# Kernel tuning notes

Hardware: AMD Instinct MI355X
Metric: run time of the kernel (lower is better)

## Reference

```python
import jax, jax.numpy as jnp
import numpy as np

B, S, D = 4, 2048, 768
H, E = 12, 64  # num_heads, head_size


def setup_inputs() -> dict:
    key = jax.random.key(0)
    ks = jax.random.split(key, 9)
    sd = 1.0 / np.sqrt(D)
    return {
        "x": jax.random.normal(ks[0], (B, S, D), dtype=jnp.float32),
        "Wq": jax.random.normal(ks[1], (H, D, E), dtype=jnp.float32) * sd,
        "bq": jax.random.normal(ks[2], (H, E), dtype=jnp.float32) * 0.02,
        "Wk": jax.random.normal(ks[3], (H, D, E), dtype=jnp.float32) * sd,
        "bk": jax.random.normal(ks[4], (H, E), dtype=jnp.float32) * 0.02,
        "Wv": jax.random.normal(ks[5], (H, D, E), dtype=jnp.float32) * sd,
        "bv": jax.random.normal(ks[6], (H, E), dtype=jnp.float32) * 0.02,
        "Wp": jax.random.normal(ks[7], (H * E, D), dtype=jnp.float32) * sd,
        "bp": jax.random.normal(ks[8], (D,), dtype=jnp.float32) * 0.02,
    }


def reference(x, Wq, bq, Wk, bk, Wv, bv, Wp, bp):
    # Batched multi-head QKV projections (replaces per-head Python loop)
    q = jnp.einsum("bsd,hde->bhse", x, Wq) + bq[None, :, None, :]
    k = jnp.einsum("bsd,hde->bhse", x, Wk) + bk[None, :, None, :]
    v = jnp.einsum("bsd,hde->bhse", x, Wv) + bv[None, :, None, :]
    scale = 1.0 / jnp.sqrt(jnp.asarray(E, dtype=x.dtype))
    # Full materialized attention matrix [B,H,S,S] as in the original module
    wei = jnp.einsum("bhqe,bhke->bhqk", q, k) * scale
    wei = jax.nn.softmax(wei, axis=-1)  # dropout=0 (eval) => identity
    out = jnp.einsum("bhqk,bhke->bhqe", wei, v)  # [B,H,S,E]
    # concat heads in head order then output projection
    out = out.transpose(0, 2, 1, 3).reshape(B, S, H * E)
    return out @ Wp + bp
```

## Files before the change

### kernel.cpp

```cpp
#include <hip/hip_runtime.h>
#include <cstddef>
#include <cstdint>

#define NB 4
#define NH 12
#define SQ 2048
#define DM 768
#define EH 64
#define MTOT (NB*SQ)
#define NQKV (NH*3*EH)

typedef __attribute__((ext_vector_type(8))) short short8;
typedef __attribute__((ext_vector_type(4))) float floatx4;

#define QSCALE 0.18033688011112042f

__device__ __forceinline__ unsigned short f2bf(float f) {
    unsigned int u = __float_as_uint(f);
    u += 0x7fffu + ((u >> 16) & 1u);
    return (unsigned short)(u >> 16);
}
__device__ __forceinline__ unsigned int pack_bf16_rhu(float lo, float hi) {
    unsigned int u0 = __float_as_uint(lo) + 0x8000u;
    unsigned int u1 = __float_as_uint(hi) + 0x8000u;
    return __builtin_amdgcn_perm(u1, u0, 0x07060302u);
}
__device__ __forceinline__ void gl_lds16(const void* g, void* l) {
    __builtin_amdgcn_global_load_lds(
        (const __attribute__((address_space(1))) unsigned int*)g,
        (__attribute__((address_space(3))) unsigned int*)l, 16, 0, 0);
}

#define CVT_A 1572864
#define CVT_B (CVT_A + 442368)
#define CVT_C (CVT_B + 147456)
#define CVT_D (CVT_C + 576)
__global__ __launch_bounds__(256) void convert_pack(
    const float* __restrict__ x,
    const float* __restrict__ Wq, const float* __restrict__ bq,
    const float* __restrict__ Wk, const float* __restrict__ bk,
    const float* __restrict__ Wv, const float* __restrict__ bv,
    const float* __restrict__ Wp,
    unsigned short* __restrict__ Xb, unsigned short* __restrict__ Wt,
    unsigned short* __restrict__ Wpt, float* __restrict__ bias_all)
{
    int t = blockIdx.x * 256 + threadIdx.x;
    if (t < CVT_A) {
        float4 v = ((const float4*)x)[t];
        ushort4 r; r.x = f2bf(v.x); r.y = f2bf(v.y); r.z = f2bf(v.z); r.w = f2bf(v.w);
        ((ushort4*)Xb)[t] = r;
    } else if (t < CVT_B) {
        int u = t - CVT_A;
        int n = u / 192, kc = (u % 192) * 4;
        int h = n / 192, rr = n % 192, wsel = rr >> 6, e = rr & 63;
        const float* W = (wsel == 0) ? Wq : ((wsel == 1) ? Wk : Wv);
        float sc = (wsel == 0) ? QSCALE : 1.0f;
        ushort4 r;
        r.x = f2bf(W[((size_t)h * DM + kc + 0) * EH + e] * sc);
        r.y = f2bf(W[((size_t)h * DM + kc + 1) * EH + e] * sc);
        r.z = f2bf(W[((size_t)h * DM + kc + 2) * EH + e] * sc);
        r.w = f2bf(W[((size_t)h * DM + kc + 3) * EH + e] * sc);
        ((ushort4*)Wt)[u] = r;
    } else if (t < CVT_C) {
        int u = t - CVT_B;
        int n = u / 192, kc = (u % 192) * 4;
        ushort4 r;
        r.x = f2bf(Wp[(size_t)(kc + 0) * DM + n]);
        r.y = f2bf(Wp[(size_t)(kc + 1) * DM + n]);
        r.z = f2bf(Wp[(size_t)(kc + 2) * DM + n]);
        r.w = f2bf(Wp[(size_t)(kc + 3) * DM + n]);
        ((ushort4*)Wpt)[u] = r;
    } else if (t < CVT_D) {
        int u = (t - CVT_C) * 4;
        #pragma unroll
        for (int j = 0; j < 4; j++) {
            int n = u + j;
            int h = n / 192, rr = n % 192, wsel = rr >> 6, e = rr & 63;
            const float* bs = (wsel == 0) ? bq : ((wsel == 1) ? bk : bv);
            bias_all[n] = bs[h * EH + e] * ((wsel == 0) ? QSCALE : 1.0f);
        }
    }
}

__global__ __launch_bounds__(256) void qkv_mfma(
    const unsigned short* __restrict__ Xb, const unsigned short* __restrict__ Wt,
    const float* __restrict__ bias_all,
    unsigned short* __restrict__ Qo, unsigned short* __restrict__ Kf,
    unsigned short* __restrict__ Vf)
{
    __shared__ unsigned short As[128 * 32];
    __shared__ unsigned short Bs[128 * 32];
    const int tid = threadIdx.x;
    const int w = tid >> 6, lane = tid & 63;
    const int l15 = lane & 15, quad = lane >> 4;
    const int wm = w & 1, wn = w >> 1;
    const int m0 = blockIdx.x * 128, n0 = blockIdx.y * 128;
    const int srow = w * 32 + (lane >> 2);
    const int pchunk = lane & 3;

    floatx4 acc[4][4];
    #pragma unroll
    for (int i = 0; i < 4; i++)
        #pragma unroll
        for (int j = 0; j < 4; j++) acc[i][j] = 0;

    for (int k0 = 0; k0 < DM; k0 += 32) {
        __syncthreads();
        #pragma unroll
        for (int c = 0; c < 2; c++) {
            int mr = srow + c * 16;
            int j = (pchunk - (mr >> 1)) & 3;
            gl_lds16(&Xb[(size_t)(m0 + mr) * DM + k0 + j * 8],
                     &As[w * 1024 + c * 512 + lane * 8]);
            gl_lds16(&Wt[(size_t)(n0 + mr) * DM + k0 + j * 8],
                     &Bs[w * 1024 + c * 512 + lane * 8]);
        }
        __syncthreads();
        short8 af[4], bf[4];
        #pragma unroll
        for (int mi = 0; mi < 4; mi++) {
            int row = wm * 64 + mi * 16 + l15;
            int pp = (quad + (row >> 1)) & 3;
            af[mi] = *(const short8*)&As[row * 32 + pp * 8];
        }
        #pragma unroll
        for (int ni = 0; ni < 4; ni++) {
            int row = wn * 64 + ni * 16 + l15;
            int pp = (quad + (row >> 1)) & 3;
            bf[ni] = *(const short8*)&Bs[row * 32 + pp * 8];
        }
        #pragma unroll
        for (int mi = 0; mi < 4; mi++)
            #pragma unroll
            for (int ni = 0; ni < 4; ni++)
                acc[mi][ni] = __builtin_amdgcn_mfma_f32_16x16x32_bf16(
                    af[mi], bf[ni], acc[mi][ni], 0, 0, 0);
    }

    const int bB = m0 >> 11;
    #pragma unroll
    for (int ni = 0; ni < 4; ni++) {
        int ntb = n0 + wn * 64 + ni * 16;
        int h = ntb / 192, rr = ntb % 192;
        int wsel = rr >> 6, e0 = rr & 63;
        float bv = bias_all[ntb + l15];
        size_t bhbase = ((size_t)bB * NH + h) * (SQ * EH);
        if (wsel == 0) {
            #pragma unroll
            for (int mi = 0; mi < 4; mi++) {
                int sb = (m0 & 2047) + wm * 64 + mi * 16 + quad * 4;
                #pragma unroll
                for (int r = 0; r < 4; r++)
                    Qo[bhbase + (size_t)(sb + r) * EH + e0 + l15] =
                        f2bf(acc[mi][ni][r] + bv);
            }
        } else if (wsel == 1) {
            int d = e0 + l15;
            int khalf = d >> 5, quad_d = (d >> 3) & 3, jj = d & 7;
            #pragma unroll
            for (int mi = 0; mi < 4; mi++) {
                int sb = (m0 & 2047) + wm * 64 + mi * 16 + quad * 4;
                int kbt = sb >> 6, nbk = (sb >> 4) & 3;
                size_t base = bhbase + (size_t)kbt * 4096 +
                    (size_t)(((nbk * 2 + khalf) * 64 + quad_d * 16 + (sb & 15))) * 8 + jj;
                #pragma unroll
                for (int r = 0; r < 4; r++)
                    Kf[base + r * 8] = f2bf(acc[mi][ni][r] + bv);
            }
        } else {
            int e = e0 + l15;
            int nbe = e >> 4;
            #pragma unroll
            for (int mi = 0; mi < 4; mi++) {
                int sb = (m0 & 2047) + wm * 64 + mi * 16 + quad * 4;
                int kbt = sb >> 6;
                int khk = (sb >> 5) & 1, qk = (sb >> 3) & 3, jb = sb & 7;
                size_t base = bhbase + (size_t)kbt * 4096 +
                    (size_t)(((nbe * 2 + khk) * 64 + qk * 16 + (e & 15))) * 8 + jb;
                ushort4 pk;
                pk.x = f2bf(acc[mi][ni][0] + bv);
                pk.y = f2bf(acc[mi][ni][1] + bv);
                pk.z = f2bf(acc[mi][ni][2] + bv);
                pk.w = f2bf(acc[mi][ni][3] + bv);
                *(ushort4*)&Vf[base] = pk;
            }
        }
    }
}

__global__ __launch_bounds__(256, 3) void attn_mfma(
    const unsigned short* __restrict__ Q, const unsigned short* __restrict__ Kf,
    const unsigned short* __restrict__ Vf, unsigned short* __restrict__ O)
{
    __shared__ unsigned short Ks[2][4096];
    __shared__ unsigned short Vs[2][4096];
    __shared__ unsigned short Pl[4][32 * 72];
    const int tid = threadIdx.x;
    const int w = tid >> 6, lane = tid & 63;
    const int l15 = lane & 15, quad = lane >> 4;
    const int bh = blockIdx.x;
    const int b = bh / NH, h = bh % NH;
    const int q0 = blockIdx.y * 128;
    unsigned short* Pw = &Pl[w][0];

    const unsigned short* Qb = Q + (size_t)bh * SQ * EH;
    const unsigned short* Kb = Kf + (size_t)bh * SQ * EH;
    const unsigned short* Vb = Vf + (size_t)bh * SQ * EH;

    short8 qf[2][2];
    #pragma unroll
    for (int qh = 0; qh < 2; qh++)
        #pragma unroll
        for (int kh = 0; kh < 2; kh++)
            qf[qh][kh] = *(const short8*)
                &Qb[(size_t)(q0 + w * 32 + qh * 16 + l15) * EH + kh * 32 + quad * 8];

    short8 ones;
    #pragma unroll
    for (int j = 0; j < 8; j++) ones[j] = (short)0x3F80;

    floatx4 o[2][4], l_acc[2];
    #pragma unroll
    for (int qh = 0; qh < 2; qh++) {
        l_acc[qh] = 0;
        #pragma unroll
        for (int nb = 0; nb < 4; nb++) o[qh][nb] = 0;
    }

    const int seg = w * 2;
    #pragma unroll
    for (int c = 0; c < 2; c++) {
        gl_lds16(&Kb[(seg + c) * 512 + lane * 8], &Ks[0][(seg + c) * 512 + lane * 8]);
        gl_lds16(&Vb[(seg + c) * 512 + lane * 8], &Vs[0][(seg + c) * 512 + lane * 8]);
    }

    #pragma unroll 2
    for (int kb = 0; kb < SQ / 64; kb++) {
        const int cur = kb & 1;
        __syncthreads();
        if (kb + 1 < SQ / 64) {
            const unsigned short* Kn = Kb + (size_t)(kb + 1) * 4096;
            const unsigned short* Vn = Vb + (size_t)(kb + 1) * 4096;
            #pragma unroll
            for (int c = 0; c < 2; c++) {
                gl_lds16(&Kn[(seg + c) * 512 + lane * 8],
                         &Ks[cur ^ 1][(seg + c) * 512 + lane * 8]);
                gl_lds16(&Vn[(seg + c) * 512 + lane * 8],
                         &Vs[cur ^ 1][(seg + c) * 512 + lane * 8]);
            }
        }
        short8 kf[4][2];
        #pragma unroll
        for (int nb = 0; nb < 4; nb++)
            #pragma unroll
            for (int kh = 0; kh < 2; kh++)
                kf[nb][kh] = *(const short8*)&Ks[cur][((nb * 2 + kh) * 64 + lane) * 8];
        floatx4 s[2][4];
        #pragma unroll
        for (int qh = 0; qh < 2; qh++)
            #pragma unroll
            for (int nb = 0; nb < 4; nb++) {
                floatx4 z = 0;
                z = __builtin_amdgcn_mfma_f32_16x16x32_bf16(kf[nb][0], qf[qh][0], z, 0, 0, 0);
                z = __builtin_amdgcn_mfma_f32_16x16x32_bf16(kf[nb][1], qf[qh][1], z, 0, 0, 0);
                s[qh][nb] = z;
            }
        #pragma unroll
        for (int qh = 0; qh < 2; qh++)
            #pragma unroll
            for (int nb = 0; nb < 4; nb++) {
                float p0 = exp2f(s[qh][nb][0]);
                float p1 = exp2f(s[qh][nb][1]);
                float p2 = exp2f(s[qh][nb][2]);
                float p3 = exp2f(s[qh][nb][3]);
                uint2 d;
                d.x = pack_bf16_rhu(p0, p1);
                d.y = pack_bf16_rhu(p2, p3);
                *(uint2*)&Pw[(qh * 16 + l15) * 72 + nb * 16 + quad * 4] = d;
            }
        short8 pa[2][2];
        #pragma unroll
        for (int qh = 0; qh < 2; qh++) {
            #pragma unroll
            for (int kh = 0; kh < 2; kh++)
                pa[qh][kh] = *(const short8*)&Pw[(qh * 16 + l15) * 72 + kh * 32 + quad * 8];
            l_acc[qh] = __builtin_amdgcn_mfma_f32_16x16x32_bf16(pa[qh][0], ones, l_acc[qh], 0, 0, 0);
            l_acc[qh] = __builtin_amdgcn_mfma_f32_16x16x32_bf16(pa[qh][1], ones, l_acc[qh], 0, 0, 0);
        }
        short8 vf[4][2];
        #pragma unroll
        for (int nb = 0; nb < 4; nb++)
            #pragma unroll
            for (int kh = 0; kh < 2; kh++)
                vf[nb][kh] = *(const short8*)&Vs[cur][((nb * 2 + kh) * 64 + lane) * 8];
        #pragma unroll
        for (int qh = 0; qh < 2; qh++)
            #pragma unroll
            for (int nb = 0; nb < 4; nb++) {
                o[qh][nb] = __builtin_amdgcn_mfma_f32_16x16x32_bf16(pa[qh][0], vf[nb][0], o[qh][nb], 0, 0, 0);
                o[qh][nb] = __builtin_amdgcn_mfma_f32_16x16x32_bf16(pa[qh][1], vf[nb][1], o[qh][nb], 0, 0, 0);
            }
    }

    #pragma unroll
    for (int qh = 0; qh < 2; qh++)
        #pragma unroll
        for (int r = 0; r < 4; r++) {
            float inv = 1.0f / l_acc[qh][r];
            int sidx = q0 + w * 32 + qh * 16 + quad * 4 + r;
            size_t base = (((size_t)b * SQ + sidx) * NH + h) * EH + l15;
            O[base +  0] = f2bf(o[qh][0][r] * inv);
            O[base + 16] = f2bf(o[qh][1][r] * inv);
            O[base + 32] = f2bf(o[qh][2][r] * inv);
            O[base + 48] = f2bf(o[qh][3][r] * inv);
        }
}

__global__ __launch_bounds__(256) void proj_mfma(
    const unsigned short* __restrict__ Ab, const unsigned short* __restrict__ Wpt,
    const float* __restrict__ bp, float* __restrict__ C)
{
    __shared__ unsigned short As[64 * 32];
    __shared__ unsigned short Bs[128 * 32];
    const int tid = threadIdx.x;
    const int w = tid >> 6, lane = tid & 63;
    const int l15 = lane & 15, quad = lane >> 4;
    const int wm = w & 1, wn = w >> 1;
    const int m0 = blockIdx.x * 64, n0 = blockIdx.y * 128;
    const int pchunk = lane & 3;

    floatx4 acc[2][4];
    #pragma unroll
    for (int i = 0; i < 2; i++)
        #pragma unroll
        for (int j = 0; j < 4; j++) acc[i][j] = 0;

    for (int k0 = 0; k0 < DM; k0 += 32) {
        __syncthreads();
        {
            int mr = w * 16 + (lane >> 2);
            int j = (pchunk - (mr >> 1)) & 3;
            gl_lds16(&Ab[(size_t)(m0 + mr) * DM + k0 + j * 8], &As[w * 512 + lane * 8]);
        }
        #pragma unroll
        for (int c = 0; c < 2; c++) {
            int nr = w * 32 + c * 16 + (lane >> 2);
            int j = (pchunk - (nr >> 1)) & 3;
            gl_lds16(&Wpt[(size_t)(n0 + nr) * DM + k0 + j * 8],
                     &Bs[w * 1024 + c * 512 + lane * 8]);
        }
        __syncthreads();
        short8 af[2], bf[4];
        #pragma unroll
        for (int mi = 0; mi < 2; mi++) {
            int row = wm * 32 + mi * 16 + l15;
            int pp = (quad + (row >> 1)) & 3;
            af[mi] = *(const short8*)&As[row * 32 + pp * 8];
        }
        #pragma unroll
        for (int ni = 0; ni < 4; ni++) {
            int row = wn * 64 + ni * 16 + l15;
            int pp = (quad + (row >> 1)) & 3;
            bf[ni] = *(const short8*)&Bs[row * 32 + pp * 8];
        }
        #pragma unroll
        for (int mi = 0; mi < 2; mi++)
            #pragma unroll
            for (int ni = 0; ni < 4; ni++)
                acc[mi][ni] = __builtin_amdgcn_mfma_f32_16x16x32_bf16(
                    af[mi], bf[ni], acc[mi][ni], 0, 0, 0);
    }

    #pragma unroll
    for (int ni = 0; ni < 4; ni++) {
        int n = n0 + wn * 64 + ni * 16 + l15;
        float bv = bp[n];
        #pragma unroll
        for (int mi = 0; mi < 2; mi++) {
            int mb = m0 + wm * 32 + mi * 16 + quad * 4;
            #pragma unroll
            for (int r = 0; r < 4; r++)
                C[(size_t)(mb + r) * DM + n] = acc[mi][ni][r] + bv;
        }
    }
}

extern "C" void kernel_launch(void* const* d_in, const int* in_sizes, int n_in,
                              void* d_out, int out_size, void* d_ws, size_t ws_size,
                              hipStream_t stream) {
    const float* x  = (const float*)d_in[0];
    const float* Wq = (const float*)d_in[1];
    const float* bq = (const float*)d_in[2];
    const float* Wk = (const float*)d_in[3];
    const float* bk = (const float*)d_in[4];
    const float* Wv = (const float*)d_in[5];
    const float* bv = (const float*)d_in[6];
    const float* Wp = (const float*)d_in[7];
    const float* bp = (const float*)d_in[8];
    float* out = (float*)d_out;

    const size_t QKV_ELEMS = (size_t)NB * NH * SQ * EH;
    unsigned short* Qb   = (unsigned short*)d_ws;
    unsigned short* Kfb  = Qb + QKV_ELEMS;
    unsigned short* Vfb  = Kfb + QKV_ELEMS;
    unsigned short* Abuf = Vfb + QKV_ELEMS;
    unsigned short* Xb   = Abuf + QKV_ELEMS;
    unsigned short* Wtb  = Xb + QKV_ELEMS;
    unsigned short* Wptb = Wtb + (size_t)NQKV * DM;
    float* bias_all      = (float*)(Wptb + (size_t)DM * DM);

    convert_pack<<<(CVT_D + 255) / 256, 256, 0, stream>>>(
        x, Wq, bq, Wk, bk, Wv, bv, Wp, Xb, Wtb, Wptb, bias_all);
    qkv_mfma<<<dim3(MTOT / 128, NQKV / 128), 256, 0, stream>>>(
        Xb, Wtb, bias_all, Qb, Kfb, Vfb);
    attn_mfma<<<dim3(NB * NH, SQ / 128), 256, 0, stream>>>(Qb, Kfb, Vfb, Abuf);
    proj_mfma<<<dim3(MTOT / 64, DM / 128), 256, 0, stream>>>(Abuf, Wptb, bp, out);
}
```

Baseline: 256.1 us.

## Keep softmax probabilities in registers by permuting V layout to match S fragments

```diff
diff --git a/kernel.cpp b/kernel.cpp
--- a/kernel.cpp
+++ b/kernel.cpp
@@ -24,6 +24,15 @@
     unsigned int u0 = __float_as_uint(lo) + 0x8000u;
     unsigned int u1 = __float_as_uint(hi) + 0x8000u;
     return __builtin_amdgcn_perm(u1, u0, 0x07060302u);
+}
+__device__ __forceinline__ short8 pack8(float a0,float a1,float a2,float a3,
+                                        float b0,float b1,float b2,float b3) {
+    union { unsigned int u[4]; short8 s; } cv;
+    cv.u[0] = pack_bf16_rhu(a0, a1);
+    cv.u[1] = pack_bf16_rhu(a2, a3);
+    cv.u[2] = pack_bf16_rhu(b0, b1);
+    cv.u[3] = pack_bf16_rhu(b2, b3);
+    return cv.s;
 }
 __device__ __forceinline__ void gl_lds16(const void* g, void* l) {
     __builtin_amdgcn_global_load_lds(
@@ -168,15 +177,15 @@
                     Kf[base + r * 8] = f2bf(acc[mi][ni][r] + bv);
             }
         } else {
-            int e = e0 + l15;
-            int nbe = e >> 4;
+            int eb = e0 >> 4;
             #pragma unroll
             for (int mi = 0; mi < 4; mi++) {
                 int sb = (m0 & 2047) + wm * 64 + mi * 16 + quad * 4;
                 int kbt = sb >> 6;
-                int khk = (sb >> 5) & 1, qk = (sb >> 3) & 3, jb = sb & 7;
+                int nbs = (sb >> 4) & 3;
+                int kh = nbs >> 1, jhi = (nbs & 1) * 4;
                 size_t base = bhbase + (size_t)kbt * 4096 +
-                    (size_t)(((nbe * 2 + khk) * 64 + qk * 16 + (e & 15))) * 8 + jb;
+                    (size_t)(((eb * 2 + kh) * 64 + quad * 16 + l15)) * 8 + jhi;
                 ushort4 pk;
                 pk.x = f2bf(acc[mi][ni][0] + bv);
                 pk.y = f2bf(acc[mi][ni][1] + bv);
@@ -194,14 +203,12 @@
 {
     __shared__ unsigned short Ks[2][4096];
     __shared__ unsigned short Vs[2][4096];
-    __shared__ unsigned short Pl[4][32 * 72];
     const int tid = threadIdx.x;
     const int w = tid >> 6, lane = tid & 63;
     const int l15 = lane & 15, quad = lane >> 4;
     const int bh = blockIdx.x;
     const int b = bh / NH, h = bh % NH;
     const int q0 = blockIdx.y * 128;
-    unsigned short* Pw = &Pl[w][0];
 
     const unsigned short* Qb = Q + (size_t)bh * SQ * EH;
     const unsigned short* Kb = Kf + (size_t)bh * SQ * EH;
@@ -265,40 +272,34 @@
                 z = __builtin_amdgcn_mfma_f32_16x16x32_bf16(kf[nb][1], qf[qh][1], z, 0, 0, 0);
                 s[qh][nb] = z;
             }
-        #pragma unroll
-        for (int qh = 0; qh < 2; qh++)
-            #pragma unroll
-            for (int nb = 0; nb < 4; nb++) {
-                float p0 = exp2f(s[qh][nb][0]);
-                float p1 = exp2f(s[qh][nb][1]);
-                float p2 = exp2f(s[qh][nb][2]);
-                float p3 = exp2f(s[qh][nb][3]);
-                uint2 d;
-                d.x = pack_bf16_rhu(p0, p1);
-                d.y = pack_bf16_rhu(p2, p3);
-                *(uint2*)&Pw[(qh * 16 + l15) * 72 + nb * 16 + quad * 4] = d;
-            }
         short8 pa[2][2];
         #pragma unroll
         for (int qh = 0; qh < 2; qh++) {
-            #pragma unroll
-            for (int kh = 0; kh < 2; kh++)
-                pa[qh][kh] = *(const short8*)&Pw[(qh * 16 + l15) * 72 + kh * 32 + quad * 8];
+            float p[4][4];
+            #pragma unroll
+            for (int nb = 0; nb < 4; nb++)
+                #pragma unroll
+                for (int r = 0; r < 4; r++)
+                    p[nb][r] = exp2f(s[qh][nb][r]);
+            pa[qh][0] = pack8(p[0][0], p[0][1], p[0][2], p[0][3],
+                              p[1][0], p[1][1], p[1][2], p[1][3]);
+            pa[qh][1] = pack8(p[2][0], p[2][1], p[2][2], p[2][3],
+                              p[3][0], p[3][1], p[3][2], p[3][3]);
             l_acc[qh] = __builtin_amdgcn_mfma_f32_16x16x32_bf16(pa[qh][0], ones, l_acc[qh], 0, 0, 0);
             l_acc[qh] = __builtin_amdgcn_mfma_f32_16x16x32_bf16(pa[qh][1], ones, l_acc[qh], 0, 0, 0);
         }
         short8 vf[4][2];
         #pragma unroll
-        for (int nb = 0; nb < 4; nb++)
+        for (int eb = 0; eb < 4; eb++)
             #pragma unroll
             for (int kh = 0; kh < 2; kh++)
-                vf[nb][kh] = *(const short8*)&Vs[cur][((nb * 2 + kh) * 64 + lane) * 8];
+                vf[eb][kh] = *(const short8*)&Vs[cur][((eb * 2 + kh) * 64 + lane) * 8];
         #pragma unroll
         for (int qh = 0; qh < 2; qh++)
             #pragma unroll
-            for (int nb = 0; nb < 4; nb++) {
-                o[qh][nb] = __builtin_amdgcn_mfma_f32_16x16x32_bf16(pa[qh][0], vf[nb][0], o[qh][nb], 0, 0, 0);
-                o[qh][nb] = __builtin_amdgcn_mfma_f32_16x16x32_bf16(pa[qh][1], vf[nb][1], o[qh][nb], 0, 0, 0);
+            for (int eb = 0; eb < 4; eb++) {
+                o[qh][eb] = __builtin_amdgcn_mfma_f32_16x16x32_bf16(pa[qh][0], vf[eb][0], o[qh][eb], 0, 0, 0);
+                o[qh][eb] = __builtin_amdgcn_mfma_f32_16x16x32_bf16(pa[qh][1], vf[eb][1], o[qh][eb], 0, 0, 0);
             }
     }
 
```

Measured after the change: 253.0 us. About the same (-1.2%).
